# Performance work log

Hardware: AMD Instinct MI355X
Metric: run time of the kernel (lower is better)

## Reference

```python
import jax, jax.numpy as jnp
import numpy as np

B, C, H, W = 4, 256, 48, 48
HEADS = 8
HALF_WIN = 8  # local_window // 2


def setup_inputs() -> dict:
    key = jax.random.key(0)
    ks = jax.random.split(key, 7)
    s = 0.02  # keep qk logits in a sane range
    return {
        "x": jax.random.normal(ks[0], (B, C, H, W), jnp.float32),
        "in_proj_w": jax.random.normal(ks[1], (3 * C, C), jnp.float32) * s,
        "in_proj_b": jax.random.normal(ks[2], (3 * C,), jnp.float32) * s,
        "out_w": jax.random.normal(ks[3], (C, C), jnp.float32) * s,
        "out_b": jax.random.normal(ks[4], (C,), jnp.float32) * s,
        "conv_w": jax.random.normal(ks[5], (C, C), jnp.float32) * s,
        "conv_b": jax.random.normal(ks[6], (C,), jnp.float32) * s,
    }


def _window_mask(Hh, Ww):
    # Additive mask [N, N]: 0 inside the local (2*half+1)^2 spatial window, -1e9 outside.
    idx = jnp.arange(Hh * Ww)
    hc, wc = idx // Ww, idx % Ww

    def axis_ok(c, L):
        lo = jnp.clip(c - HALF_WIN, 0, L)
        hi = jnp.clip(c + HALF_WIN + 1, 0, L)
        return (c[None, :] >= lo[:, None]) & (c[None, :] < hi[:, None])

    inside = axis_ok(hc, Hh) & axis_ok(wc, Ww)
    return jnp.where(inside, 0.0, -1e9).astype(jnp.float32)


def reference(x, in_proj_w, in_proj_b, out_w, out_b, conv_w, conv_b):
    b, c, h, w = x.shape
    n = h * w
    hd = c // HEADS
    xf = x.reshape(b, c, n).transpose(0, 2, 1)  # [B, N, C]

    qkv = xf @ in_proj_w.T + in_proj_b  # [B, N, 3C]
    q, k, v = jnp.split(qkv, 3, axis=-1)

    def heads(t):  # [B, N, C] -> [B, H, N, hd]
        return t.reshape(b, n, HEADS, hd).transpose(0, 2, 1, 3)

    q, k, v = heads(q), heads(k), heads(v)

    mask = _window_mask(h, w)  # [N, N]
    scores = jnp.einsum('bhqd,bhkd->bhqk', q, k) / np.float32(np.sqrt(hd)) + mask
    attn = jax.nn.softmax(scores, axis=-1)
    o = jnp.einsum('bhqk,bhkd->bhqd', attn, v)  # [B, H, N, hd]
    o = o.transpose(0, 2, 1, 3).reshape(b, n, c)
    o = o @ out_w.T + out_b  # MHA out_proj

    res = o.transpose(0, 2, 1).reshape(b, c, h, w) + x
    out = jnp.einsum('oc,bchw->bohw', conv_w, res) + conv_b[None, :, None, None]
    return jax.nn.relu(out)
```

## Files before the change

kernel.cpp:

```cpp
#include <hip/hip_runtime.h>
#include <math.h>

#define BB 4
#define CC 256
#define HH 48
#define WI 48
#define NN (HH*WI)
#define NHEAD 8
#define HD 32
#define PLANE ((size_t)NN*HD)
#define BUF   (BB*NHEAD*NN*HD)

typedef unsigned short u16;
typedef __attribute__((ext_vector_type(8))) short bf16x8;
typedef __attribute__((ext_vector_type(4))) float f32x4;

__device__ inline u16 f2bf(float f) {
  union { float f; unsigned u; } v; v.f = f;
  unsigned r = v.u + 0x7FFFu + ((v.u >> 16) & 1u);
  return (u16)(r >> 16);
}
__device__ inline u16 f2bf_rna(float f) {
  union { float f; unsigned u; } v; v.f = f;
  return (u16)((v.u + 0x8000u) >> 16);
}

__global__ __launch_bounds__(256) void prep_kernel(
    const float* __restrict__ x, const float* __restrict__ w1,
    const float* __restrict__ w2, const float* __restrict__ w3,
    u16* __restrict__ XT, u16* __restrict__ W1b,
    u16* __restrict__ W2b, u16* __restrict__ W3b) {
  __shared__ float T[32][36];
  const int bx = blockIdx.x;
  const int t = threadIdx.x;
  if (bx < 2304) {
    const int n0 = (bx % 72) * 32, c0 = ((bx / 72) & 7) * 32, b = bx / 576;
    const int c = t >> 3, n4 = (t & 7) * 4;
    *(float4*)&T[c][n4] = *(const float4*)&x[((size_t)b * CC + c0 + c) * NN + n0 + n4];
    __syncthreads();
    const int nn = t >> 3, c4 = (t & 7) * 4;
    ushort4 o;
    o.x = f2bf(T[c4 + 0][nn]); o.y = f2bf(T[c4 + 1][nn]);
    o.z = f2bf(T[c4 + 2][nn]); o.w = f2bf(T[c4 + 3][nn]);
    *(ushort4*)&XT[((size_t)b * NN + n0 + nn) * CC + c0 + c4] = o;
  } else {
    const int i = ((bx - 2304) * 256 + t) * 4;
    const float* src; u16* dst; int off;
    if (i < 196608)      { src = w1; dst = W1b; off = i; }
    else if (i < 262144) { src = w2; dst = W2b; off = i - 196608; }
    else                 { src = w3; dst = W3b; off = i - 262144; }
    float4 v = *(const float4*)&src[off];
    ushort4 o = {f2bf(v.x), f2bf(v.y), f2bf(v.z), f2bf(v.w)};
    *(ushort4*)&dst[off] = o;
  }
}

__device__ __forceinline__ void gemm_core(
    const u16* __restrict__ act, const u16* __restrict__ wb,
    int m0, int j0, u16 (&As)[128][40], u16 (&Ws)[128][40],
    f32x4 (&acc)[4][4], int tid) {
  const int lane = tid & 63, ll = lane & 15, lh = lane >> 4;
  const int wv = tid >> 6;
  const int wm = (wv >> 1) << 6, wj = (wv & 1) << 6;
  const int r_ = tid >> 1;
  const int kh = (tid & 1) << 4;
  for (int k0 = 0; k0 < CC; k0 += 32) {
    __syncthreads();
    bf16x8 a0 = *(const bf16x8*)&act[(size_t)(m0 + r_) * CC + k0 + kh];
    bf16x8 a1 = *(const bf16x8*)&act[(size_t)(m0 + r_) * CC + k0 + kh + 8];
    bf16x8 w0 = *(const bf16x8*)&wb[(size_t)(j0 + r_) * CC + k0 + kh];
    bf16x8 w1 = *(const bf16x8*)&wb[(size_t)(j0 + r_) * CC + k0 + kh + 8];
    *(bf16x8*)&As[r_][kh]     = a0;
    *(bf16x8*)&As[r_][kh + 8] = a1;
    *(bf16x8*)&Ws[r_][kh]     = w0;
    *(bf16x8*)&Ws[r_][kh + 8] = w1;
    __syncthreads();
    bf16x8 af[4], bfv[4];
#pragma unroll
    for (int s = 0; s < 4; ++s) {
      af[s]  = *(const bf16x8*)&As[wm + s * 16 + ll][lh * 8];
      bfv[s] = *(const bf16x8*)&Ws[wj + s * 16 + ll][lh * 8];
    }
#pragma unroll
    for (int ms = 0; ms < 4; ++ms)
#pragma unroll
      for (int js = 0; js < 4; ++js)
        acc[ms][js] = __builtin_amdgcn_mfma_f32_16x16x32_bf16(af[ms], bfv[js], acc[ms][js], 0, 0, 0);
  }
}

__device__ __forceinline__ void gemm_core64(
    const u16* __restrict__ act, const u16* __restrict__ wb,
    int m0, int j0, u16 (&As)[64][40], u16 (&Ws)[64][40],
    f32x4 (&acc)[2][2], int tid) {
  const int lane = tid & 63, ll = lane & 15, lh = lane >> 4;
  const int wv = tid >> 6;
  const int wm = (wv >> 1) << 5, wj = (wv & 1) << 5;
  const bool isW = (tid >= 128);
  const int r_ = (tid & 127) >> 1;
  const int kh = (tid & 1) << 4;
  const u16* src = isW ? &wb[(size_t)(j0 + r_) * CC + kh]
                       : &act[(size_t)(m0 + r_) * CC + kh];
  u16* dst = isW ? &Ws[r_][kh] : &As[r_][kh];
  for (int k0 = 0; k0 < CC; k0 += 32) {
    __syncthreads();
    bf16x8 v0 = *(const bf16x8*)(src + k0);
    bf16x8 v1 = *(const bf16x8*)(src + k0 + 8);
    *(bf16x8*)dst       = v0;
    *(bf16x8*)(dst + 8) = v1;
    __syncthreads();
    bf16x8 af[2], bfv[2];
#pragma unroll
    for (int s = 0; s < 2; ++s) {
      af[s]  = *(const bf16x8*)&As[wm + s * 16 + ll][lh * 8];
      bfv[s] = *(const bf16x8*)&Ws[wj + s * 16 + ll][lh * 8];
    }
#pragma unroll
    for (int ms = 0; ms < 2; ++ms)
#pragma unroll
      for (int js = 0; js < 2; ++js)
        acc[ms][js] = __builtin_amdgcn_mfma_f32_16x16x32_bf16(af[ms], bfv[js], acc[ms][js], 0, 0, 0);
  }
}

__global__ __launch_bounds__(256) void qkv_gemm(
    const u16* __restrict__ XT, const u16* __restrict__ W1b,
    const float* __restrict__ bias,
    u16* __restrict__ Qb, u16* __restrict__ Kb, u16* __restrict__ VTb) {
  __shared__ u16 As[128][40];
  __shared__ u16 Ws[128][40];
  const int tid = threadIdx.x;
  const int m0 = blockIdx.x * 128, j0 = blockIdx.y * 128;
  f32x4 acc[4][4] = {};
  gemm_core(XT, W1b, m0, j0, As, Ws, acc, tid);

  const int lane = tid & 63, ll = lane & 15, lh = lane >> 4;
  const int wv = tid >> 6;
  const int wm = (wv >> 1) << 6, wj = (wv & 1) << 6;
  const int part = blockIdx.y >> 1;
  const int b = m0 / NN, n0 = m0 % NN;
#pragma unroll
  for (int js = 0; js < 4; ++js) {
    const int j = j0 + wj + js * 16 + ll;
    const float bj = bias[j];
    const int head = (j >> 5) & 7, d = j & 31;
#pragma unroll
    for (int ms = 0; ms < 4; ++ms) {
      const int nb = n0 + wm + ms * 16 + (lh << 2);
      if (part == 2) {
        ushort4 v = {f2bf(acc[ms][js][0] + bj), f2bf(acc[ms][js][1] + bj),
                     f2bf(acc[ms][js][2] + bj), f2bf(acc[ms][js][3] + bj)};
        *(ushort4*)&VTb[(((size_t)b * NHEAD + head) * HD + d) * NN + nb] = v;
      } else {
        u16* dst = (part == 0 ? Qb : Kb) + ((size_t)b * NHEAD + head) * PLANE;
#pragma unroll
        for (int r = 0; r < 4; ++r)
          dst[(size_t)(nb + r) * HD + d] = f2bf(acc[ms][js][r] + bj);
      }
    }
  }
}

__global__ __launch_bounds__(256) void attn_mfma(
    const u16* __restrict__ Qb, const u16* __restrict__ Kb,
    const u16* __restrict__ VTb, u16* __restrict__ Ob) {
  __shared__ u16 Ks[2][64][32];
  __shared__ u16 VTs[2][32][72];
  __shared__ u16 Ps[4][16][40];
  const int bid0 = blockIdx.x;
  const int bid  = (bid0 & 7) * 144 + (bid0 >> 3);
  const int tile = bid % 36;
  const int head = (bid / 36) & 7;
  const int b    = bid / 288;
  const int th0 = (tile / 3) * 4, tw0 = (tile % 3) * 16;
  const int tid = threadIdx.x;
  const int wv = tid >> 6, lane = tid & 63;
  const int lh = lane >> 4, ll = lane & 15;
  const size_t plane = ((size_t)b * NHEAD + head) * PLANE;

  const int wlo = max(0, tw0 - 8);
  const int nw  = min(WI, tw0 + 24) - wlo;
  const int rlo = max(0, th0 - 8), rhi = min(HH, th0 + 12);

  const int qh = th0 + wv;
  const bf16x8 qfrag = *(const bf16x8*)&Qb[plane + (size_t)(qh * WI + tw0 + ll) * HD + lh * 8];

  int qw_r[4];
  float cb0[4], cb1[4];
  const int wk0 = wlo + ll;
  const int wk1 = wlo + 16 + ll;
#pragma unroll
  for (int r = 0; r < 4; ++r) {
    qw_r[r] = tw0 + (lh << 2) + r;
    cb0[r] = (abs(wk0 - qw_r[r]) <= 8) ? 0.0f : -30000.0f;
    cb1[r] = (wk1 < WI && abs(wk1 - qw_r[r]) <= 8) ? 0.0f : -30000.0f;
  }

  f32x4 o0 = {0.f, 0.f, 0.f, 0.f}, o1 = {0.f, 0.f, 0.f, 0.f};
  const f32x4 zf = {0.f, 0.f, 0.f, 0.f};
  float lsum[4] = {0.f, 0.f, 0.f, 0.f};
  const int sk_slot = tid >> 2, sk_d = (tid & 3) * 8;
  const int sk_rr = sk_slot >> 5;
  const int sk_c  = min(sk_slot & 31, nw - 1);
  const int sv_d = tid >> 3, sv_s = (tid & 7) * 8;
  const int sv_rr = sv_s >> 5;
  const int sv_c  = min(sv_s & 31, nw - 1);
  const float C2 = 0.25501651847296056f;
  const int nch = (rhi - rlo) >> 1;

  {
    bf16x8 kv = *(const bf16x8*)&Kb[plane + (size_t)((rlo + sk_rr) * WI + wlo + sk_c) * HD + sk_d];
    bf16x8 vv = *(const bf16x8*)&VTb[plane + (size_t)sv_d * NN + (rlo + sv_rr) * WI + wlo + sv_c];
    *(bf16x8*)&Ks[0][sk_slot][sk_d] = kv;
    *(bf16x8*)&VTs[0][sv_d][sv_s] = vv;
  }

  int cur = 0;
  for (int c = 0; c < nch; ++c) {
    const int hk2 = rlo + (c << 1);
    bf16x8 nkv, nvv;
    const bool more = (c + 1 < nch);
    if (more) {
      nkv = *(const bf16x8*)&Kb[plane + (size_t)((hk2 + 2 + sk_rr) * WI + wlo + sk_c) * HD + sk_d];
      nvv = *(const bf16x8*)&VTb[plane + (size_t)sv_d * NN + (hk2 + 2 + sv_rr) * WI + wlo + sv_c];
    }
    __syncthreads();
#pragma unroll
    for (int rr = 0; rr < 2; ++rr) {
      const int hk = hk2 + rr;
      if (hk >= qh - 8 && hk <= qh + 8) {
        const int sb = rr << 5;
        __builtin_amdgcn_s_setprio(1);
        const bf16x8 k0 = *(const bf16x8*)&Ks[cur][sb + ll][lh * 8];
        const bf16x8 k1 = *(const bf16x8*)&Ks[cur][sb + 16 + ll][lh * 8];
        f32x4 s0 = __builtin_amdgcn_mfma_f32_16x16x32_bf16(qfrag, k0, zf, 0, 0, 0);
        f32x4 s1 = __builtin_amdgcn_mfma_f32_16x16x32_bf16(qfrag, k1, zf, 0, 0, 0);
#pragma unroll
        for (int r = 0; r < 4; ++r) {
          float e0 = exp2f(fmaf(s0[r], C2, cb0[r]));
          float e1 = exp2f(fmaf(s1[r], C2, cb1[r]));
          lsum[r] += e0 + e1;
          Ps[wv][(lh << 2) + r][ll]      = f2bf_rna(e0);
          Ps[wv][(lh << 2) + r][16 + ll] = f2bf_rna(e1);
        }
        const bf16x8 pa = *(const bf16x8*)&Ps[wv][ll][lh * 8];
        const bf16x8 v0 = *(const bf16x8*)&VTs[cur][ll][sb + lh * 8];
        const bf16x8 v1 = *(const bf16x8*)&VTs[cur][16 + ll][sb + lh * 8];
        o0 = __builtin_amdgcn_mfma_f32_16x16x32_bf16(pa, v0, o0, 0, 0, 0);
        o1 = __builtin_amdgcn_mfma_f32_16x16x32_bf16(pa, v1, o1, 0, 0, 0);
        __builtin_amdgcn_s_setprio(0);
      }
    }
    if (more) {
      *(bf16x8*)&Ks[cur ^ 1][sk_slot][sk_d] = nkv;
      *(bf16x8*)&VTs[cur ^ 1][sv_d][sv_s] = nvv;
    }
    cur ^= 1;
  }

#pragma unroll
  for (int r = 0; r < 4; ++r) {
    float s = lsum[r];
    s += __shfl_xor(s, 1); s += __shfl_xor(s, 2);
    s += __shfl_xor(s, 4); s += __shfl_xor(s, 8);
    const float inv = 1.0f / s;
    const size_t row = ((size_t)b * NN + qh * WI + qw_r[r]) * CC + head * HD;
    Ob[row + ll]      = f2bf(o0[r] * inv);
    Ob[row + 16 + ll] = f2bf(o1[r] * inv);
  }
}

__global__ __launch_bounds__(256) void outproj_gemm(
    const u16* __restrict__ Ob, const u16* __restrict__ W2b,
    const float* __restrict__ bias, const float* __restrict__ x,
    u16* __restrict__ RESb) {
  __shared__ u16 As[64][40];
  __shared__ u16 Ws[64][40];
  const int tid = threadIdx.x;
  const int m0 = blockIdx.x * 64, j0 = blockIdx.y * 64;
  f32x4 acc[2][2] = {};
  gemm_core64(Ob, W2b, m0, j0, As, Ws, acc, tid);

  const int lane = tid & 63, ll = lane & 15, lh = lane >> 4;
  const int wv = tid >> 6;
  const int wm = (wv >> 1) << 5, wj = (wv & 1) << 5;
  const int b = m0 / NN, n0 = m0 % NN;
#pragma unroll
  for (int js = 0; js < 2; ++js) {
    const int j = j0 + wj + js * 16 + ll;
    const float bj = bias[j];
#pragma unroll
    for (int ms = 0; ms < 2; ++ms) {
      const int nb = n0 + wm + ms * 16 + (lh << 2);
      float4 xr = *(const float4*)&x[((size_t)b * CC + j) * NN + nb];
      float rr[4] = {acc[ms][js][0] + bj + xr.x, acc[ms][js][1] + bj + xr.y,
                     acc[ms][js][2] + bj + xr.z, acc[ms][js][3] + bj + xr.w};
#pragma unroll
      for (int r = 0; r < 4; ++r)
        RESb[(size_t)(m0 + wm + ms * 16 + (lh << 2) + r) * CC + j] = f2bf(rr[r]);
    }
  }
}

__global__ __launch_bounds__(256) void conv_gemm(
    const u16* __restrict__ RESb, const u16* __restrict__ W3b,
    const float* __restrict__ bias, float* __restrict__ out) {
  __shared__ u16 As[64][40];
  __shared__ u16 Ws[64][40];
  const int tid = threadIdx.x;
  const int m0 = blockIdx.x * 64, j0 = blockIdx.y * 64;
  f32x4 acc[2][2] = {};
  gemm_core64(RESb, W3b, m0, j0, As, Ws, acc, tid);

  const int lane = tid & 63, ll = lane & 15, lh = lane >> 4;
  const int wv = tid >> 6;
  const int wm = (wv >> 1) << 5, wj = (wv & 1) << 5;
  const int b = m0 / NN, n0 = m0 % NN;
#pragma unroll
  for (int js = 0; js < 2; ++js) {
    const int j = j0 + wj + js * 16 + ll;
    const float bj = bias[j];
#pragma unroll
    for (int ms = 0; ms < 2; ++ms) {
      const int nb = n0 + wm + ms * 16 + (lh << 2);
      float4 v;
      v.x = fmaxf(acc[ms][js][0] + bj, 0.0f);
      v.y = fmaxf(acc[ms][js][1] + bj, 0.0f);
      v.z = fmaxf(acc[ms][js][2] + bj, 0.0f);
      v.w = fmaxf(acc[ms][js][3] + bj, 0.0f);
      *(float4*)&out[((size_t)b * CC + j) * NN + nb] = v;
    }
  }
}

extern "C" void kernel_launch(void* const* d_in, const int* in_sizes, int n_in,
                              void* d_out, int out_size, void* d_ws, size_t ws_size,
                              hipStream_t stream) {
  const float* x         = (const float*)d_in[0];
  const float* in_proj_w = (const float*)d_in[1];
  const float* in_proj_b = (const float*)d_in[2];
  const float* out_w     = (const float*)d_in[3];
  const float* out_b     = (const float*)d_in[4];
  const float* conv_w    = (const float*)d_in[5];
  const float* conv_b    = (const float*)d_in[6];
  float* out = (float*)d_out;

  u16* wsb = (u16*)d_ws;
  u16* XT   = wsb;
  u16* Qb   = wsb + (size_t)BUF;
  u16* Kb   = wsb + (size_t)2 * BUF;
  u16* VTb  = wsb + (size_t)3 * BUF;
  u16* Ob   = wsb + (size_t)4 * BUF;
  u16* RESb = wsb + (size_t)5 * BUF;
  u16* W1b  = wsb + (size_t)6 * BUF;
  u16* W2b  = W1b + 196608;
  u16* W3b  = W2b + 65536;

  prep_kernel<<<dim3(2624), dim3(256), 0, stream>>>(x, in_proj_w, out_w, conv_w,
                                                    XT, W1b, W2b, W3b);
  qkv_gemm<<<dim3(72, 6), dim3(256), 0, stream>>>(XT, W1b, in_proj_b, Qb, Kb, VTb);
  attn_mfma<<<dim3(1152), dim3(256), 0, stream>>>(Qb, Kb, VTb, Ob);
  outproj_gemm<<<dim3(144, 4), dim3(256), 0, stream>>>(Ob, W2b, out_b, x, RESb);
  conv_gemm<<<dim3(144, 4), dim3(256), 0, stream>>>(RESb, W3b, conv_b, out);
}
```

Baseline: 58.17 us.

## Fold out-projection into conv weights and fuse final GEMMs into one kernel

Precomputes W3·W2 and W3·b2+b3 in the prep kernel so the out-projection and the 1x1 conv collapse into a single GEMM over [O | XT] with concatenated K. This removes one kernel launch and the RESb intermediate round-trip through memory. The cost is a slightly larger K in the final GEMM, a small weight-product GEMM computed every call, and different bf16 rounding because the combined weight and the residual path (XT in bf16) are quantized separately.

```diff
diff --git a/kernel.cpp b/kernel.cpp
--- a/kernel.cpp
+++ b/kernel.cpp
@@ -28,12 +28,14 @@
 __global__ __launch_bounds__(256) void prep_kernel(
     const float* __restrict__ x, const float* __restrict__ w1,
     const float* __restrict__ w2, const float* __restrict__ w3,
-    u16* __restrict__ XT, u16* __restrict__ W1b,
-    u16* __restrict__ W2b, u16* __restrict__ W3b) {
-  __shared__ float T[32][36];
+    const float* __restrict__ b2, const float* __restrict__ b3,
+    u16* __restrict__ XT, u16* __restrict__ W1b, u16* __restrict__ W3b,
+    u16* __restrict__ W32b, float* __restrict__ b23) {
+  __shared__ char smem[10240];
   const int bx = blockIdx.x;
   const int t = threadIdx.x;
   if (bx < 2304) {
+    float (*T)[36] = (float(*)[36])smem;
     const int n0 = (bx % 72) * 32, c0 = ((bx / 72) & 7) * 32, b = bx / 576;
     const int c = t >> 3, n4 = (t & 7) * 4;
     *(float4*)&T[c][n4] = *(const float4*)&x[((size_t)b * CC + c0 + c) * NN + n0 + n4];
@@ -43,15 +45,76 @@
     o.x = f2bf(T[c4 + 0][nn]); o.y = f2bf(T[c4 + 1][nn]);
     o.z = f2bf(T[c4 + 2][nn]); o.w = f2bf(T[c4 + 3][nn]);
     *(ushort4*)&XT[((size_t)b * NN + n0 + nn) * CC + c0 + c4] = o;
-  } else {
+  } else if (bx < 2560) {
     const int i = ((bx - 2304) * 256 + t) * 4;
     const float* src; u16* dst; int off;
-    if (i < 196608)      { src = w1; dst = W1b; off = i; }
-    else if (i < 262144) { src = w2; dst = W2b; off = i - 196608; }
-    else                 { src = w3; dst = W3b; off = i - 262144; }
+    if (i < 196608) { src = w1; dst = W1b; off = i; }
+    else            { src = w3; dst = W3b; off = i - 196608; }
     float4 v = *(const float4*)&src[off];
     ushort4 o = {f2bf(v.x), f2bf(v.y), f2bf(v.z), f2bf(v.w)};
     *(ushort4*)&dst[off] = o;
+  } else if (bx < 2576) {
+    u16 (*As)[40] = (u16(*)[40])smem;
+    u16 (*Ws)[40] = (u16(*)[40])&smem[5120];
+    const int bb = bx - 2560;
+    const int m0 = (bb & 3) * 64, n0 = (bb >> 2) * 64;
+    const int lane = t & 63, ll = lane & 15, lh = lane >> 4;
+    const int wv = t >> 6;
+    const int wm = (wv >> 1) << 5, wj = (wv & 1) << 5;
+    const bool isW = (t >= 128);
+    const int r_ = (t & 127) >> 1;
+    const int kh = (t & 1) << 4;
+    f32x4 acc[2][2] = {};
+    for (int k0 = 0; k0 < 256; k0 += 32) {
+      __syncthreads();
+      if (!isW) {
+        const float* s = &w3[(size_t)(m0 + r_) * 256 + k0 + kh];
+#pragma unroll
+        for (int i = 0; i < 16; i += 4) {
+          float4 v = *(const float4*)(s + i);
+          As[r_][kh + i]     = f2bf(v.x);
+          As[r_][kh + i + 1] = f2bf(v.y);
+          As[r_][kh + i + 2] = f2bf(v.z);
+          As[r_][kh + i + 3] = f2bf(v.w);
+        }
+      } else {
+#pragma unroll
+        for (int i = 0; i < 16; ++i)
+          Ws[r_][kh + i] = f2bf(w2[(size_t)(k0 + kh + i) * 256 + n0 + r_]);
+      }
+      __syncthreads();
+      bf16x8 af[2], bfv[2];
+#pragma unroll
+      for (int s = 0; s < 2; ++s) {
+        af[s]  = *(const bf16x8*)&As[wm + s * 16 + ll][lh * 8];
+        bfv[s] = *(const bf16x8*)&Ws[wj + s * 16 + ll][lh * 8];
+      }
+#pragma unroll
+      for (int ms = 0; ms < 2; ++ms)
+#pragma unroll
+        for (int js = 0; js < 2; ++js)
+          acc[ms][js] = __builtin_amdgcn_mfma_f32_16x16x32_bf16(af[ms], bfv[js], acc[ms][js], 0, 0, 0);
+    }
+#pragma unroll
+    for (int js = 0; js < 2; ++js) {
+      const int j = n0 + wj + js * 16 + ll;
+#pragma unroll
+      for (int ms = 0; ms < 2; ++ms) {
+        const int row = m0 + wm + ms * 16 + (lh << 2);
+#pragma unroll
+        for (int r = 0; r < 4; ++r)
+          W32b[(size_t)(row + r) * 256 + j] = f2bf(acc[ms][js][r]);
+      }
+    }
+  } else {
+    float s = b3[t];
+    const float* row = &w3[(size_t)t * 256];
+    for (int c = 0; c < 256; c += 4) {
+      float4 wv = *(const float4*)(row + c);
+      float4 bv = *(const float4*)(b2 + c);
+      s += wv.x * bv.x + wv.y * bv.y + wv.z * bv.z + wv.w * bv.w;
+    }
+    b23[t] = s;
   }
 }
 
@@ -270,16 +333,17 @@
   }
 }
 
-__global__ __launch_bounds__(256) void outproj_gemm(
-    const u16* __restrict__ Ob, const u16* __restrict__ W2b,
-    const float* __restrict__ bias, const float* __restrict__ x,
-    u16* __restrict__ RESb) {
+__global__ __launch_bounds__(256) void final_gemm(
+    const u16* __restrict__ Ob, const u16* __restrict__ XT,
+    const u16* __restrict__ W32b, const u16* __restrict__ W3b,
+    const float* __restrict__ b23, float* __restrict__ out) {
   __shared__ u16 As[64][40];
   __shared__ u16 Ws[64][40];
   const int tid = threadIdx.x;
   const int m0 = blockIdx.x * 64, j0 = blockIdx.y * 64;
   f32x4 acc[2][2] = {};
-  gemm_core64(Ob, W2b, m0, j0, As, Ws, acc, tid);
+  gemm_core64(Ob, W32b, m0, j0, As, Ws, acc, tid);
+  gemm_core64(XT, W3b,  m0, j0, As, Ws, acc, tid);
 
   const int lane = tid & 63, ll = lane & 15, lh = lane >> 4;
   const int wv = tid >> 6;
@@ -288,38 +352,7 @@
 #pragma unroll
   for (int js = 0; js < 2; ++js) {
     const int j = j0 + wj + js * 16 + ll;
-    const float bj = bias[j];
-#pragma unroll
-    for (int ms = 0; ms < 2; ++ms) {
-      const int nb = n0 + wm + ms * 16 + (lh << 2);
-      float4 xr = *(const float4*)&x[((size_t)b * CC + j) * NN + nb];
-      float rr[4] = {acc[ms][js][0] + bj + xr.x, acc[ms][js][1] + bj + xr.y,
-                     acc[ms][js][2] + bj + xr.z, acc[ms][js][3] + bj + xr.w};
-#pragma unroll
-      for (int r = 0; r < 4; ++r)
-        RESb[(size_t)(m0 + wm + ms * 16 + (lh << 2) + r) * CC + j] = f2bf(rr[r]);
-    }
-  }
-}
-
-__global__ __launch_bounds__(256) void conv_gemm(
-    const u16* __restrict__ RESb, const u16* __restrict__ W3b,
-    const float* __restrict__ bias, float* __restrict__ out) {
-  __shared__ u16 As[64][40];
-  __shared__ u16 Ws[64][40];
-  const int tid = threadIdx.x;
-  const int m0 = blockIdx.x * 64, j0 = blockIdx.y * 64;
-  f32x4 acc[2][2] = {};
-  gemm_core64(RESb, W3b, m0, j0, As, Ws, acc, tid);
-
-  const int lane = tid & 63, ll = lane & 15, lh = lane >> 4;
-  const int wv = tid >> 6;
-  const int wm = (wv >> 1) << 5, wj = (wv & 1) << 5;
-  const int b = m0 / NN, n0 = m0 % NN;
-#pragma unroll
-  for (int js = 0; js < 2; ++js) {
-    const int j = j0 + wj + js * 16 + ll;
-    const float bj = bias[j];
+    const float bj = b23[j];
 #pragma unroll
     for (int ms = 0; ms < 2; ++ms) {
       const int nb = n0 + wm + ms * 16 + (lh << 2);
@@ -351,15 +384,14 @@
   u16* Kb   = wsb + (size_t)2 * BUF;
   u16* VTb  = wsb + (size_t)3 * BUF;
   u16* Ob   = wsb + (size_t)4 * BUF;
-  u16* RESb = wsb + (size_t)5 * BUF;
-  u16* W1b  = wsb + (size_t)6 * BUF;
-  u16* W2b  = W1b + 196608;
-  u16* W3b  = W2b + 65536;
-
-  prep_kernel<<<dim3(2624), dim3(256), 0, stream>>>(x, in_proj_w, out_w, conv_w,
-                                                    XT, W1b, W2b, W3b);
+  u16* W1b  = wsb + (size_t)5 * BUF;
+  u16* W3b  = W1b + 196608;
+  u16* W32b = W3b + 65536;
+  float* b23 = (float*)(W32b + 65536);
+
+  prep_kernel<<<dim3(2577), dim3(256), 0, stream>>>(
+      x, in_proj_w, out_w, conv_w, out_b, conv_b, XT, W1b, W3b, W32b, b23);
   qkv_gemm<<<dim3(72, 6), dim3(256), 0, stream>>>(XT, W1b, in_proj_b, Qb, Kb, VTb);
   attn_mfma<<<dim3(1152), dim3(256), 0, stream>>>(Qb, Kb, VTb, Ob);
-  outproj_gemm<<<dim3(144, 4), dim3(256), 0, stream>>>(Ob, W2b, out_b, x, RESb);
-  conv_gemm<<<dim3(144, 4), dim3(256), 0, stream>>>(RESb, W3b, conv_b, out);
-}
+  final_gemm<<<dim3(144, 4), dim3(256), 0, stream>>>(Ob, XT, W32b, W3b, b23, out);
+}
```

New measurement: 60.92 us. +4.7%, slower.
